# Kernel tuning notes

Measured on AMD Instinct MI355X. Metric: run time of the kernel, lower is better.

Reference implementation:

```python
import jax, jax.numpy as jnp
import numpy as np

DIM = 768
N_HEADS = 12
HEAD_DIM = DIM // N_HEADS
MAX_REL = 3  # hardcoded in the module


def setup_inputs() -> dict:
    key = jax.random.key(0)
    ks = jax.random.split(key, 10)
    B, L = 4, 1024
    def xavier(k, shape):
        fan_in, fan_out = shape[-2], shape[-1]
        a = jnp.sqrt(6.0 / (fan_in + fan_out))
        return jax.random.uniform(k, shape, jnp.float32, -a, a)
    return {
        "query": jax.random.normal(ks[0], (B, L, DIM), jnp.float32),
        "key":   jax.random.normal(ks[1], (B, L, DIM), jnp.float32),
        "value": jax.random.normal(ks[2], (B, L, DIM), jnp.float32),
        "Wq": xavier(ks[3], (DIM, DIM)),
        "Wk": xavier(ks[4], (DIM, DIM)),
        "Wv": xavier(ks[5], (DIM, DIM)),
        "Wproj": xavier(ks[6], (DIM, DIM)),
        "b_proj": jnp.zeros((DIM,), jnp.float32),
        "rel_k_table": xavier(ks[7], (2 * MAX_REL + 1, HEAD_DIM)),
        "rel_v_table": xavier(ks[8], (2 * MAX_REL + 1, HEAD_DIM)),
    }


def _rel_embed(table, len_q, len_k):
    # [len_q, len_k, head_dim] gathered from clipped relative distances
    dist = jnp.arange(len_k)[None, :] - jnp.arange(len_q)[:, None]
    idx = jnp.clip(dist, -MAX_REL, MAX_REL) + MAX_REL
    return table[idx]


def reference(query, key, value, Wq, Wk, Wv, Wproj, b_proj, rel_k_table, rel_v_table):
    B, Lq, _ = query.shape
    Lk = key.shape[1]
    H, hd = N_HEADS, HEAD_DIM
    scale = hd ** (-0.5)

    q = query @ Wq.T                      # [B, Lq, D]
    k = key @ Wk.T                        # [B, Lk, D]
    v = value @ Wv.T                      # [B, Lk, D]

    qh = q.reshape(B, Lq, H, hd).transpose(0, 2, 1, 3)   # [B,H,Lq,hd]
    kh = k.reshape(B, Lk, H, hd).transpose(0, 2, 1, 3)
    vh = v.reshape(B, Lk, H, hd).transpose(0, 2, 1, 3)

    # content-content scores
    attn1 = jnp.einsum('bhqd,bhkd->bhqk', qh, kh)
    # content-relative-position scores
    rk = _rel_embed(rel_k_table, Lq, Lk)                  # [Lq,Lk,hd]
    attn2 = jnp.einsum('bhqd,qkd->bhqk', qh, rk)
    # NOTE: original code DIVIDES by scale (= hd**-0.5), i.e. multiplies by sqrt(hd)
    attn = (attn1 + attn2) / scale
    attn = jax.nn.softmax(attn, axis=-1)                  # [B,H,Lq,Lk]

    w1 = jnp.einsum('bhqk,bhkd->bhqd', attn, vh)
    rv = _rel_embed(rel_v_table, Lq, Lk)                  # [Lq,Lk,hd]
    w2 = jnp.einsum('bhqk,qkd->bhqd', attn, rv)

    x = (w1 + w2).transpose(0, 2, 1, 3).reshape(B, Lq, H * hd)
    x = x @ Wproj.T + b_proj
    return (x, attn)
```

## Files before the change

### kernel.cpp

```cpp
#include <hip/hip_runtime.h>

#define DIMM 768
#define NH 12
#define HD 64
#define LSEQ 1024
#define BATCH 4
#define NXE 3145728
#define NWE 589824

typedef __bf16 bf16x8 __attribute__((ext_vector_type(8)));
typedef float f32x4 __attribute__((ext_vector_type(4)));
typedef unsigned short u16;

static __device__ __forceinline__ u16 f2bf(float f) {
  unsigned u = __builtin_bit_cast(unsigned, f);
  u += 0x7fffu + ((u >> 16) & 1u);
  return (u16)(u >> 16);
}
static __device__ __forceinline__ float bf2f(u16 h) {
  unsigned u = ((unsigned)h) << 16;
  return __builtin_bit_cast(float, u);
}
static __device__ __forceinline__ bf16x8 ld8bf(const u16* p) {
  uint4 u = *(const uint4*)p;
  return __builtin_bit_cast(bf16x8, u);
}
#define MFMA(a, b, c) __builtin_amdgcn_mfma_f32_16x16x32_bf16(a, b, c, 0, 0, 0)
#define GLL(g, s)                                                      \
  __builtin_amdgcn_global_load_lds(                                    \
      (const __attribute__((address_space(1))) void*)(g),              \
      (__attribute__((address_space(3))) void*)(s), 16, 0, 0)

__global__ __launch_bounds__(256) void convert(
    const float* __restrict__ q_in, const float* __restrict__ k_in,
    const float* __restrict__ v_in, const float* __restrict__ Wq,
    const float* __restrict__ Wk, const float* __restrict__ Wv,
    const float* __restrict__ Wp, u16* __restrict__ AqH, u16* __restrict__ AqL,
    u16* __restrict__ AkH, u16* __restrict__ AkL, u16* __restrict__ Av,
    u16* __restrict__ WqH, u16* __restrict__ WqL, u16* __restrict__ WkH,
    u16* __restrict__ WkL, u16* __restrict__ Wvr, u16* __restrict__ Wpr) {
  long i = ((long)blockIdx.x * 256 + threadIdx.x) * 4;
  const float* src;
  u16 *dh, *dl = nullptr;
  long off;
  if (i < NXE) { src = q_in; dh = AqH; dl = AqL; off = i; }
  else if (i < 2L * NXE) { src = k_in; dh = AkH; dl = AkL; off = i - NXE; }
  else if (i < 3L * NXE) { src = v_in; dh = Av; off = i - 2L * NXE; }
  else {
    long j = i - 3L * NXE;
    int which = (int)(j / NWE);
    off = j % NWE;
    if (which == 0) { src = Wq; dh = WqH; dl = WqL; }
    else if (which == 1) { src = Wk; dh = WkH; dl = WkL; }
    else if (which == 2) { src = Wv; dh = Wvr; }
    else { src = Wp; dh = Wpr; }
  }
  float4 v = *(const float4*)(src + off);
  ushort4 h;
  h.x = f2bf(v.x); h.y = f2bf(v.y); h.z = f2bf(v.z); h.w = f2bf(v.w);
  *(ushort4*)(dh + off) = h;
  if (dl) {
    ushort4 lo;
    lo.x = f2bf(v.x - bf2f(h.x)); lo.y = f2bf(v.y - bf2f(h.y));
    lo.z = f2bf(v.z - bf2f(h.z)); lo.w = f2bf(v.w - bf2f(h.w));
    *(ushort4*)(dl + off) = lo;
  }
}

__global__ __launch_bounds__(256, 3) void gemm_multi(
    int mode0, const u16* __restrict__ AqH, const u16* __restrict__ AqL,
    const u16* __restrict__ AkH, const u16* __restrict__ AkL,
    const u16* __restrict__ Av, const u16* __restrict__ WqH,
    const u16* __restrict__ WqL, const u16* __restrict__ WkH,
    const u16* __restrict__ WkL, const u16* __restrict__ Wvr,
    const u16* __restrict__ Wpr, const u16* __restrict__ wbuf,
    u16* __restrict__ qhi, u16* __restrict__ qlo, u16* __restrict__ khi,
    u16* __restrict__ klo, u16* __restrict__ vT, float* __restrict__ outp,
    const float* __restrict__ bias) {
  __shared__ u16 sAh[128 * 32], sAl[128 * 32];
  __shared__ u16 sBh[128 * 32], sBl[128 * 32];
  const int mode = mode0 + blockIdx.z;
  const u16 *Ah, *Al = nullptr, *Bh, *Bl = nullptr;
  if (mode == 0) { Ah = AqH; Al = AqL; Bh = WqH; Bl = WqL; }
  else if (mode == 1) { Ah = AkH; Al = AkL; Bh = WkH; Bl = WkL; }
  else if (mode == 2) { Ah = Av; Bh = Wvr; }
  else { Ah = wbuf; Bh = Wpr; }
  const int t = threadIdx.x, w = t >> 6, l = t & 63;
  const int quad = l >> 4, l15 = l & 15;
  const int m0 = blockIdx.x * 128, n0 = blockIdx.y * 128;
  const int wm = (w >> 1) * 64, wn = (w & 1) * 64;
  const int srow = t >> 2, scol = (t & 3) * 8;
  const u16* gA = Ah + (m0 + srow) * DIMM + scol;
  const u16* gB = Bh + (n0 + srow) * DIMM + scol;
  u16* lA = sAh + w * 512;
  u16* lB = sBh + w * 512;
  f32x4 acc[4][4] = {};
  if (mode < 2) {
    const u16* gAl = Al + (m0 + srow) * DIMM + scol;
    const u16* gBl = Bl + (n0 + srow) * DIMM + scol;
    u16* lAl = sAl + w * 512;
    u16* lBl = sBl + w * 512;
    for (int k0 = 0; k0 < DIMM; k0 += 32) {
      GLL(gA + k0, lA);
      GLL(gA + 64 * DIMM + k0, lA + 2048);
      GLL(gAl + k0, lAl);
      GLL(gAl + 64 * DIMM + k0, lAl + 2048);
      GLL(gB + k0, lB);
      GLL(gB + 64 * DIMM + k0, lB + 2048);
      GLL(gBl + k0, lBl);
      GLL(gBl + 64 * DIMM + k0, lBl + 2048);
      __syncthreads();
      bf16x8 ah[4], bh[4], xl[4];
#pragma unroll
      for (int i = 0; i < 4; ++i)
        ah[i] = __builtin_bit_cast(
            bf16x8, *(const uint4*)(sAh + (wm + i * 16 + l15) * 32 + quad * 8));
#pragma unroll
      for (int j = 0; j < 4; ++j)
        bh[j] = __builtin_bit_cast(
            bf16x8, *(const uint4*)(sBh + (wn + j * 16 + l15) * 32 + quad * 8));
#pragma unroll
      for (int i = 0; i < 4; ++i)
#pragma unroll
        for (int j = 0; j < 4; ++j) acc[i][j] = MFMA(ah[i], bh[j], acc[i][j]);
#pragma unroll
      for (int i = 0; i < 4; ++i)
        xl[i] = __builtin_bit_cast(
            bf16x8, *(const uint4*)(sAl + (wm + i * 16 + l15) * 32 + quad * 8));
#pragma unroll
      for (int i = 0; i < 4; ++i)
#pragma unroll
        for (int j = 0; j < 4; ++j) acc[i][j] = MFMA(xl[i], bh[j], acc[i][j]);
#pragma unroll
      for (int j = 0; j < 4; ++j)
        xl[j] = __builtin_bit_cast(
            bf16x8, *(const uint4*)(sBl + (wn + j * 16 + l15) * 32 + quad * 8));
#pragma unroll
      for (int i = 0; i < 4; ++i)
#pragma unroll
        for (int j = 0; j < 4; ++j) acc[i][j] = MFMA(ah[i], xl[j], acc[i][j]);
      __syncthreads();
    }
  } else {
    for (int k0 = 0; k0 < DIMM; k0 += 32) {
      GLL(gA + k0, lA);
      GLL(gA + 64 * DIMM + k0, lA + 2048);
      GLL(gB + k0, lB);
      GLL(gB + 64 * DIMM + k0, lB + 2048);
      __syncthreads();
      bf16x8 ah[4], bh[4];
#pragma unroll
      for (int i = 0; i < 4; ++i)
        ah[i] = __builtin_bit_cast(
            bf16x8, *(const uint4*)(sAh + (wm + i * 16 + l15) * 32 + quad * 8));
#pragma unroll
      for (int j = 0; j < 4; ++j)
        bh[j] = __builtin_bit_cast(
            bf16x8, *(const uint4*)(sBh + (wn + j * 16 + l15) * 32 + quad * 8));
#pragma unroll
      for (int i = 0; i < 4; ++i)
#pragma unroll
        for (int j = 0; j < 4; ++j) acc[i][j] = MFMA(ah[i], bh[j], acc[i][j]);
      __syncthreads();
    }
  }
  u16* oh = (mode == 0) ? qhi : khi;
  u16* ol = (mode == 0) ? qlo : klo;
#pragma unroll
  for (int i = 0; i < 4; ++i)
#pragma unroll
    for (int j = 0; j < 4; ++j)
#pragma unroll
      for (int r = 0; r < 4; ++r) {
        int grow = m0 + wm + i * 16 + quad * 4 + r;
        int gcol = n0 + wn + j * 16 + l15;
        float c = acc[i][j][r];
        int b = grow >> 10, ll = grow & 1023, h = gcol >> 6, d = gcol & 63;
        if (mode < 2) {
          int idx = ((b * NH + h) * LSEQ + ll) * HD + d;
          u16 hi = f2bf(c);
          oh[idx] = hi;
          ol[idx] = f2bf(c - bf2f(hi));
        } else if (mode == 2) {
          vT[((b * NH + h) * HD + d) * LSEQ + ll] = f2bf(c);
        } else {
          outp[grow * DIMM + gcol] = c + bias[gcol];
        }
      }
}

__global__ __launch_bounds__(256, 3) void attn_core(
    const u16* __restrict__ qhi, const u16* __restrict__ qlo,
    const u16* __restrict__ khi, const u16* __restrict__ klo,
    const u16* __restrict__ vT, const float* __restrict__ relk,
    const float* __restrict__ relv, float* __restrict__ attn_out,
    u16* __restrict__ wbuf) {
  __shared__ __align__(16) u16 uni[16 * 1032];
  __shared__ float qrel[16][7];
  __shared__ float arel[16][7];
  __shared__ float rvt[7][64];
  __shared__ float red[4][16][4];

  const int Lb = blockIdx.x + 64 * (blockIdx.y + NH * blockIdx.z);
  const int flat = (Lb & 7) * 384 + (Lb >> 3);
  const int qt = flat & 63, h = (flat >> 6) % NH, b = flat / (64 * NH);
  const int q0 = qt * 16;
  const int tid = threadIdx.x, wave = tid >> 6, lane = tid & 63;
  const int quad = lane >> 4, l15 = lane & 15;
  const int bhd = b * NH + h;

  const int rs = tid >> 3;
  const int cg = (tid & 7) ^ (rs & 7);
  const u16* gh = khi + (bhd * LSEQ + rs) * HD + cg * 8;
  const u16* gl = klo + (bhd * LSEQ + rs) * HD + cg * 8;
  u16* sb = uni + wave * 512;
  const int rowA = wave * 16 + l15;
  const int sw = rowA & 7;
  const int s0 = (rowA * 8 + (quad ^ sw)) * 8;
  const int s1 = (rowA * 8 + ((quad + 4) ^ sw)) * 8;

#define STAGE_K(c, bufsel)                                             \
  do {                                                                 \
    const u16* ghc_ = gh + (c) * (64 * HD);                            \
    const u16* glc_ = gl + (c) * (64 * HD);                            \
    u16* nb_ = sb + (bufsel) * 8192;                                   \
    GLL(ghc_, nb_);                                \
    GLL(ghc_ + 32 * HD, nb_ + 2048);               \
    GLL(glc_, nb_ + 4096);                         \
    GLL(glc_ + 32 * HD, nb_ + 6144);               \
  } while (0)

  STAGE_K(0, 0);

  for (int t = tid; t < 7 * HD; t += 256) rvt[t >> 6][t & 63] = relv[t];
  if (tid < 112) {
    int q = tid / 7, rr = tid % 7;
    const u16* qp = qhi + (bhd * LSEQ + q0 + q) * HD;
    const u16* lp = qlo + (bhd * LSEQ + q0 + q) * HD;
    const float* tp = relk + rr * HD;
    float s = 0.f;
#pragma unroll
    for (int d8 = 0; d8 < HD; d8 += 8) {
      uint4 uh = *(const uint4*)(qp + d8);
      uint4 ul = *(const uint4*)(lp + d8);
      float4 t0 = *(const float4*)(tp + d8);
      float4 t1 = *(const float4*)(tp + d8 + 4);
      unsigned hh[4] = {uh.x, uh.y, uh.z, uh.w};
      unsigned lv[4] = {ul.x, ul.y, ul.z, ul.w};
      float tv[8] = {t0.x, t0.y, t0.z, t0.w, t1.x, t1.y, t1.z, t1.w};
#pragma unroll
      for (int m = 0; m < 4; ++m) {
        s += (bf2f((u16)(hh[m] & 0xffff)) + bf2f((u16)(lv[m] & 0xffff))) * tv[2 * m];
        s += (bf2f((u16)(hh[m] >> 16)) + bf2f((u16)(lv[m] >> 16))) * tv[2 * m + 1];
      }
    }
    qrel[q][rr] = s;
    arel[q][rr] = 0.f;
  }

  f32x4 sc[16];
  {
    const int qbase = (bhd * LSEQ + q0 + l15) * HD + quad * 8;
    bf16x8 ah0 = ld8bf(qhi + qbase);
    bf16x8 ah1 = ld8bf(qhi + qbase + 32);
    bf16x8 al0 = ld8bf(qlo + qbase);
    bf16x8 al1 = ld8bf(qlo + qbase + 32);
    __syncthreads();
    for (int c = 0; c < 16; ++c) {
      if (c < 15) STAGE_K(c + 1, (c + 1) & 1);
      const u16* cur = uni + (c & 1) * 8192;
      bf16x8 kh0 = ld8bf(cur + s0);
      bf16x8 kh1 = ld8bf(cur + s1);
      bf16x8 kl0 = ld8bf(cur + 4096 + s0);
      bf16x8 kl1 = ld8bf(cur + 4096 + s1);
      f32x4 e = {}, f = {};
      e = MFMA(ah0, kh0, e);
      f = MFMA(ah1, kh1, f);
      e = MFMA(ah0, kl0, e);
      f = MFMA(ah1, kl1, f);
      e = MFMA(al0, kh0, e);
      f = MFMA(al1, kh1, f);
      sc[c] = e + f;
      __syncthreads();
    }
  }

  const int colbase = wave * 16 + l15;
  const int dbase = colbase - q0 - quad * 4;
  float mrow[4] = {-3.4e38f, -3.4e38f, -3.4e38f, -3.4e38f};
#pragma unroll
  for (int c = 0; c < 16; ++c)
#pragma unroll
    for (int r = 0; r < 4; ++r) {
      int d = dbase + c * 64 - r;
      int ri = d < -3 ? 0 : (d > 3 ? 6 : d + 3);
      float s = (sc[c][r] + qrel[quad * 4 + r][ri]) * 8.0f;
      sc[c][r] = s;
      mrow[r] = fmaxf(mrow[r], s);
    }
#pragma unroll
  for (int m = 1; m <= 8; m <<= 1)
#pragma unroll
    for (int r = 0; r < 4; ++r) mrow[r] = fmaxf(mrow[r], __shfl_xor(mrow[r], m));
  if (l15 < 4) {
    float mv = l15 == 0 ? mrow[0] : l15 == 1 ? mrow[1] : l15 == 2 ? mrow[2] : mrow[3];
    red[0][quad * 4 + l15][wave] = mv;
  }
  __syncthreads();
  float mx[4];
#pragma unroll
  for (int r = 0; r < 4; ++r) {
    int row = quad * 4 + r;
    mx[r] = fmaxf(fmaxf(red[0][row][0], red[0][row][1]),
                  fmaxf(red[0][row][2], red[0][row][3]));
  }

  float sum[4] = {}, s0a[4] = {}, s6a[4] = {};
#pragma unroll
  for (int c = 0; c < 16; ++c)
#pragma unroll
    for (int r = 0; r < 4; ++r) {
      float e = __expf(sc[c][r] - mx[r]);
      sc[c][r] = e;
      int d = dbase + c * 64 - r;
      sum[r] += e;
      if (d <= -3) s0a[r] += e;
      if (d >= 3) s6a[r] += e;
    }
#pragma unroll
  for (int m = 1; m <= 8; m <<= 1)
#pragma unroll
    for (int r = 0; r < 4; ++r) {
      sum[r] += __shfl_xor(sum[r], m);
      s0a[r] += __shfl_xor(s0a[r], m);
      s6a[r] += __shfl_xor(s6a[r], m);
    }
  if (l15 < 4) {
    int row = quad * 4 + l15;
    float sv = l15 == 0 ? sum[0] : l15 == 1 ? sum[1] : l15 == 2 ? sum[2] : sum[3];
    float a0 = l15 == 0 ? s0a[0] : l15 == 1 ? s0a[1] : l15 == 2 ? s0a[2] : s0a[3];
    float a6 = l15 == 0 ? s6a[0] : l15 == 1 ? s6a[1] : l15 == 2 ? s6a[2] : s6a[3];
    red[1][row][wave] = sv;
    red[2][row][wave] = a0;
    red[3][row][wave] = a6;
  }
  __syncthreads();
  float rn[4];
#pragma unroll
  for (int r = 0; r < 4; ++r) {
    int row = quad * 4 + r;
    float s = red[1][row][0] + red[1][row][1] + red[1][row][2] + red[1][row][3];
    rn[r] = 1.0f / s;
    if (wave == 0 && l15 == 0) {
      float t0 = red[2][row][0] + red[2][row][1] + red[2][row][2] + red[2][row][3];
      float t6 = red[3][row][0] + red[3][row][1] + red[3][row][2] + red[3][row][3];
      arel[row][0] = t0 * rn[r];
      arel[row][6] = t6 * rn[r];
    }
  }

#pragma unroll
  for (int c = 0; c < 16; ++c) {
    int col = colbase + c * 64;
#pragma unroll
    for (int r = 0; r < 4; ++r) {
      int row = quad * 4 + r;
      float p = sc[c][r] * rn[r];
      uni[row * 1032 + col] = f2bf(p);
      int d = dbase + c * 64 - r;
      if (d >= -2 && d <= 2) arel[row][d + 3] = p;
    }
  }
  __syncthreads();

  {
    float* aob = attn_out + ((size_t)(bhd * LSEQ + q0)) * LSEQ;
#pragma unroll
    for (int row = 0; row < 16; ++row) {
      uint2 u = *(const uint2*)&uni[row * 1032 + tid * 4];
      float4 f = {bf2f((u16)(u.x & 0xffff)), bf2f((u16)(u.x >> 16)),
                  bf2f((u16)(u.y & 0xffff)), bf2f((u16)(u.y >> 16))};
      *(float4*)(aob + row * LSEQ + tid * 4) = f;
    }
  }

  {
    const u16* vb = vT + (bhd * HD + wave * 16 + l15) * LSEQ;
    f32x4 acc0 = {}, acc1 = {};
#pragma unroll 4
    for (int kk = 0; kk < LSEQ; kk += 64) {
      int ak = kk + quad * 8;
      bf16x8 aP0 = __builtin_bit_cast(bf16x8, *(const uint4*)&uni[l15 * 1032 + ak]);
      bf16x8 bV0 = ld8bf(vb + ak);
      acc0 = MFMA(aP0, bV0, acc0);
      bf16x8 aP1 = __builtin_bit_cast(bf16x8, *(const uint4*)&uni[l15 * 1032 + ak + 32]);
      bf16x8 bV1 = ld8bf(vb + ak + 32);
      acc1 = MFMA(aP1, bV1, acc1);
    }
    f32x4 acc = acc0 + acc1;
    const int col = wave * 16 + l15;
#pragma unroll
    for (int r = 0; r < 4; ++r) {
      int row = quad * 4 + r;
      float w2 = 0.f;
#pragma unroll
      for (int t = 0; t < 7; ++t) w2 += arel[row][t] * rvt[t][col];
      wbuf[(b * LSEQ + q0 + row) * DIMM + h * HD + col] = f2bf(acc[r] + w2);
    }
  }
#undef STAGE_K
}

extern "C" void kernel_launch(void* const* d_in, const int* in_sizes, int n_in,
                              void* d_out, int out_size, void* d_ws, size_t ws_size,
                              hipStream_t stream) {
  const float* q_in = (const float*)d_in[0];
  const float* k_in = (const float*)d_in[1];
  const float* v_in = (const float*)d_in[2];
  const float* Wq = (const float*)d_in[3];
  const float* Wk = (const float*)d_in[4];
  const float* Wv = (const float*)d_in[5];
  const float* Wp = (const float*)d_in[6];
  const float* bias = (const float*)d_in[7];
  const float* relk = (const float*)d_in[8];
  const float* relv = (const float*)d_in[9];
  float* out = (float*)d_out;

  u16* p = (u16*)d_ws;
  u16 *AqH = p, *AqL = AqH + NXE, *AkH = AqL + NXE, *AkL = AkH + NXE,
      *Av = AkL + NXE;
  u16 *WqH = Av + NXE, *WqL = WqH + NWE, *WkH = WqL + NWE, *WkL = WkH + NWE,
      *Wvr = WkL + NWE, *Wpr = Wvr + NWE;
  u16 *qhi = Wpr + NWE, *qlo = qhi + NXE, *khi = qlo + NXE, *klo = khi + NXE,
      *vT = klo + NXE, *wbuf = vT + NXE;

  convert<<<(3 * NXE + 4 * NWE) / 1024, 256, 0, stream>>>(
      q_in, k_in, v_in, Wq, Wk, Wv, Wp, AqH, AqL, AkH, AkL, Av, WqH, WqL, WkH,
      WkL, Wvr, Wpr);
  gemm_multi<<<dim3(32, 6, 3), 256, 0, stream>>>(
      0, AqH, AqL, AkH, AkL, Av, WqH, WqL, WkH, WkL, Wvr, Wpr, wbuf, qhi, qlo,
      khi, klo, vT, out, bias);
  attn_core<<<dim3(64, NH, BATCH), 256, 0, stream>>>(
      qhi, qlo, khi, klo, vT, relk, relv, out + NXE, wbuf);
  gemm_multi<<<dim3(32, 6, 1), 256, 0, stream>>>(
      3, AqH, AqL, AkH, AkL, Av, WqH, WqL, WkH, WkL, Wvr, Wpr, wbuf, qhi, qlo,
      khi, klo, vT, out, bias);
}
```

Before: 436.1 us.

## Halve GEMM M-tile and overlap next-tile global loads with MFMA compute

The projection GEMM now uses 64x128 tiles instead of 128x128, doubling the grid and raising the launch-bounds occupancy hint from 3 to 4 blocks per SM. The K loop is restructured so operands are read from LDS into registers, followed by a barrier, after which the next K-slice's global-to-LDS loads are issued before the MFMAs run, overlapping memory with compute. The cost is less data reuse per block, more total global traffic for the B operand, and more register pressure from holding hi/lo fragments simultaneously.

```diff
diff --git a/kernel.cpp b/kernel.cpp
--- a/kernel.cpp
+++ b/kernel.cpp
@@ -67,7 +67,7 @@
   }
 }
 
-__global__ __launch_bounds__(256, 3) void gemm_multi(
+__global__ __launch_bounds__(256, 4) void gemm_multi(
     int mode0, const u16* __restrict__ AqH, const u16* __restrict__ AqL,
     const u16* __restrict__ AkH, const u16* __restrict__ AkL,
     const u16* __restrict__ Av, const u16* __restrict__ WqH,
@@ -77,7 +77,7 @@
     u16* __restrict__ qhi, u16* __restrict__ qlo, u16* __restrict__ khi,
     u16* __restrict__ klo, u16* __restrict__ vT, float* __restrict__ outp,
     const float* __restrict__ bias) {
-  __shared__ u16 sAh[128 * 32], sAl[128 * 32];
+  __shared__ u16 sAh[64 * 32], sAl[64 * 32];
   __shared__ u16 sBh[128 * 32], sBl[128 * 32];
   const int mode = mode0 + blockIdx.z;
   const u16 *Ah, *Al = nullptr, *Bh, *Bl = nullptr;
@@ -87,87 +87,91 @@
   else { Ah = wbuf; Bh = Wpr; }
   const int t = threadIdx.x, w = t >> 6, l = t & 63;
   const int quad = l >> 4, l15 = l & 15;
-  const int m0 = blockIdx.x * 128, n0 = blockIdx.y * 128;
-  const int wm = (w >> 1) * 64, wn = (w & 1) * 64;
+  const int m0 = blockIdx.x * 64, n0 = blockIdx.y * 128;
+  const int wm = (w & 1) * 32, wn = (w >> 1) * 64;
   const int srow = t >> 2, scol = (t & 3) * 8;
   const u16* gA = Ah + (m0 + srow) * DIMM + scol;
   const u16* gB = Bh + (n0 + srow) * DIMM + scol;
+  const u16* gAl = (mode < 2) ? Al + (m0 + srow) * DIMM + scol : nullptr;
+  const u16* gBl = (mode < 2) ? Bl + (n0 + srow) * DIMM + scol : nullptr;
   u16* lA = sAh + w * 512;
   u16* lB = sBh + w * 512;
-  f32x4 acc[4][4] = {};
+  u16* lAl = sAl + w * 512;
+  u16* lBl = sBl + w * 512;
+  f32x4 acc[2][4] = {};
+
+#define STAGE_G(k0)                                                    \
+  do {                                                                 \
+    GLL(gA + (k0), lA);                                                \
+    GLL(gB + (k0), lB);                                                \
+    GLL(gB + 64 * DIMM + (k0), lB + 2048);                             \
+    if (mode < 2) {                                                    \
+      GLL(gAl + (k0), lAl);                                            \
+      GLL(gBl + (k0), lBl);                                            \
+      GLL(gBl + 64 * DIMM + (k0), lBl + 2048);                         \
+    }                                                                  \
+  } while (0)
+
+  STAGE_G(0);
   if (mode < 2) {
-    const u16* gAl = Al + (m0 + srow) * DIMM + scol;
-    const u16* gBl = Bl + (n0 + srow) * DIMM + scol;
-    u16* lAl = sAl + w * 512;
-    u16* lBl = sBl + w * 512;
     for (int k0 = 0; k0 < DIMM; k0 += 32) {
-      GLL(gA + k0, lA);
-      GLL(gA + 64 * DIMM + k0, lA + 2048);
-      GLL(gAl + k0, lAl);
-      GLL(gAl + 64 * DIMM + k0, lAl + 2048);
-      GLL(gB + k0, lB);
-      GLL(gB + 64 * DIMM + k0, lB + 2048);
-      GLL(gBl + k0, lBl);
-      GLL(gBl + 64 * DIMM + k0, lBl + 2048);
       __syncthreads();
-      bf16x8 ah[4], bh[4], xl[4];
-#pragma unroll
-      for (int i = 0; i < 4; ++i)
+      bf16x8 ah[2], al[2], bh[4], bl[4];
+#pragma unroll
+      for (int i = 0; i < 2; ++i) {
+        ah[i] = __builtin_bit_cast(
+            bf16x8, *(const uint4*)(sAh + (wm + i * 16 + l15) * 32 + quad * 8));
+        al[i] = __builtin_bit_cast(
+            bf16x8, *(const uint4*)(sAl + (wm + i * 16 + l15) * 32 + quad * 8));
+      }
+#pragma unroll
+      for (int j = 0; j < 4; ++j) {
+        bh[j] = __builtin_bit_cast(
+            bf16x8, *(const uint4*)(sBh + (wn + j * 16 + l15) * 32 + quad * 8));
+        bl[j] = __builtin_bit_cast(
+            bf16x8, *(const uint4*)(sBl + (wn + j * 16 + l15) * 32 + quad * 8));
+      }
+      __syncthreads();
+      if (k0 + 32 < DIMM) STAGE_G(k0 + 32);
+#pragma unroll
+      for (int i = 0; i < 2; ++i)
+#pragma unroll
+        for (int j = 0; j < 4; ++j) acc[i][j] = MFMA(ah[i], bh[j], acc[i][j]);
+#pragma unroll
+      for (int i = 0; i < 2; ++i)
+#pragma unroll
+        for (int j = 0; j < 4; ++j) acc[i][j] = MFMA(al[i], bh[j], acc[i][j]);
+#pragma unroll
+      for (int i = 0; i < 2; ++i)
+#pragma unroll
+        for (int j = 0; j < 4; ++j) acc[i][j] = MFMA(ah[i], bl[j], acc[i][j]);
+    }
+  } else {
+    for (int k0 = 0; k0 < DIMM; k0 += 32) {
+      __syncthreads();
+      bf16x8 ah[2], bh[4];
+#pragma unroll
+      for (int i = 0; i < 2; ++i)
         ah[i] = __builtin_bit_cast(
             bf16x8, *(const uint4*)(sAh + (wm + i * 16 + l15) * 32 + quad * 8));
 #pragma unroll
       for (int j = 0; j < 4; ++j)
         bh[j] = __builtin_bit_cast(
             bf16x8, *(const uint4*)(sBh + (wn + j * 16 + l15) * 32 + quad * 8));
-#pragma unroll
-      for (int i = 0; i < 4; ++i)
+      __syncthreads();
+      if (k0 + 32 < DIMM) STAGE_G(k0 + 32);
+#pragma unroll
+      for (int i = 0; i < 2; ++i)
 #pragma unroll
         for (int j = 0; j < 4; ++j) acc[i][j] = MFMA(ah[i], bh[j], acc[i][j]);
-#pragma unroll
-      for (int i = 0; i < 4; ++i)
-        xl[i] = __builtin_bit_cast(
-            bf16x8, *(const uint4*)(sAl + (wm + i * 16 + l15) * 32 + quad * 8));
-#pragma unroll
-      for (int i = 0; i < 4; ++i)
-#pragma unroll
-        for (int j = 0; j < 4; ++j) acc[i][j] = MFMA(xl[i], bh[j], acc[i][j]);
-#pragma unroll
-      for (int j = 0; j < 4; ++j)
-        xl[j] = __builtin_bit_cast(
-            bf16x8, *(const uint4*)(sBl + (wn + j * 16 + l15) * 32 + quad * 8));
-#pragma unroll
-      for (int i = 0; i < 4; ++i)
-#pragma unroll
-        for (int j = 0; j < 4; ++j) acc[i][j] = MFMA(ah[i], xl[j], acc[i][j]);
-      __syncthreads();
-    }
-  } else {
-    for (int k0 = 0; k0 < DIMM; k0 += 32) {
-      GLL(gA + k0, lA);
-      GLL(gA + 64 * DIMM + k0, lA + 2048);
-      GLL(gB + k0, lB);
-      GLL(gB + 64 * DIMM + k0, lB + 2048);
-      __syncthreads();
-      bf16x8 ah[4], bh[4];
-#pragma unroll
-      for (int i = 0; i < 4; ++i)
-        ah[i] = __builtin_bit_cast(
-            bf16x8, *(const uint4*)(sAh + (wm + i * 16 + l15) * 32 + quad * 8));
-#pragma unroll
-      for (int j = 0; j < 4; ++j)
-        bh[j] = __builtin_bit_cast(
-            bf16x8, *(const uint4*)(sBh + (wn + j * 16 + l15) * 32 + quad * 8));
-#pragma unroll
-      for (int i = 0; i < 4; ++i)
-#pragma unroll
-        for (int j = 0; j < 4; ++j) acc[i][j] = MFMA(ah[i], bh[j], acc[i][j]);
-      __syncthreads();
-    }
-  }
+    }
+  }
+#undef STAGE_G
+
   u16* oh = (mode == 0) ? qhi : khi;
   u16* ol = (mode == 0) ? qlo : klo;
 #pragma unroll
-  for (int i = 0; i < 4; ++i)
+  for (int i = 0; i < 2; ++i)
 #pragma unroll
     for (int j = 0; j < 4; ++j)
 #pragma unroll
@@ -437,12 +441,12 @@
   convert<<<(3 * NXE + 4 * NWE) / 1024, 256, 0, stream>>>(
       q_in, k_in, v_in, Wq, Wk, Wv, Wp, AqH, AqL, AkH, AkL, Av, WqH, WqL, WkH,
       WkL, Wvr, Wpr);
-  gemm_multi<<<dim3(32, 6, 3), 256, 0, stream>>>(
+  gemm_multi<<<dim3(64, 6, 3), 256, 0, stream>>>(
       0, AqH, AqL, AkH, AkL, Av, WqH, WqL, WkH, WkL, Wvr, Wpr, wbuf, qhi, qlo,
       khi, klo, vT, out, bias);
   attn_core<<<dim3(64, NH, BATCH), 256, 0, stream>>>(
       qhi, qlo, khi, klo, vT, relk, relv, out + NXE, wbuf);
-  gemm_multi<<<dim3(32, 6, 1), 256, 0, stream>>>(
+  gemm_multi<<<dim3(64, 6, 1), 256, 0, stream>>>(
       3, AqH, AqL, AkH, AkL, Av, WqH, WqL, WkH, WkL, Wvr, Wpr, wbuf, qhi, qlo,
       khi, klo, vT, out, bias);
 }
```

Result: no change. 439.6 us (+0.8%).
